# Kernel tuning notes

Measured on AMD Instinct MI355X. Metric: run time of the kernel, lower is better.

## Reference

```python
import jax, jax.numpy as jnp
import numpy as np

B, S, D = 2, 2048, 1024
NH, HD = 16, 64
MLP = 4096
EPS = 1e-6  # flax nnx.RMSNorm default epsilon


def rms_norm(x, scale):
    var = jnp.mean(jnp.square(x.astype(jnp.float32)), axis=-1, keepdims=True)
    return (x * jax.lax.rsqrt(var + EPS)).astype(x.dtype) * scale


def setup_inputs() -> dict:
    key = jax.random.key(0)
    ks = jax.random.split(key, 16)
    lin = lambda k, fin, fout: jax.random.normal(k, (fin, fout), jnp.float32) / np.sqrt(fin)
    x = jax.random.normal(ks[0], (B, S, D), jnp.float32)
    # causal mask [b, s, s]
    mask = jnp.broadcast_to(jnp.tril(jnp.ones((S, S), jnp.bool_))[None], (B, S, S))
    return {
        "x": x,
        "mask": mask,
        "attn_norm_scale": jnp.ones((D,), jnp.float32),
        "q_w": lin(ks[1], D, D), "q_b": jnp.zeros((D,), jnp.float32),
        "k_w": lin(ks[2], D, D), "k_b": jnp.zeros((D,), jnp.float32),
        "v_w": lin(ks[3], D, D), "v_b": jnp.zeros((D,), jnp.float32),
        "o_w": lin(ks[4], D, D), "o_b": jnp.zeros((D,), jnp.float32),
        "ffn_norm_scale": jnp.ones((D,), jnp.float32),
        "gate_w": lin(ks[5], D, MLP), "gate_b": jnp.zeros((MLP,), jnp.float32),
        "up_w": lin(ks[6], D, MLP), "up_b": jnp.zeros((MLP,), jnp.float32),
        "down_w": lin(ks[7], MLP, D), "down_b": jnp.zeros((D,), jnp.float32),
    }


def reference(x, mask, attn_norm_scale, q_w, q_b, k_w, k_b, v_w, v_b, o_w, o_b,
              ffn_norm_scale, gate_w, gate_b, up_w, up_b, down_w, down_b):
    b, s, d = x.shape
    h = rms_norm(x, attn_norm_scale)
    q = (h @ q_w + q_b).reshape(b, s, NH, HD)
    k = (h @ k_w + k_b).reshape(b, s, NH, HD)
    v = (h @ v_w + v_b).reshape(b, s, NH, HD)
    scale = jnp.float32(HD) ** -0.5
    logits = jnp.einsum('bsnh,btnh->bnst', q, k) * scale  # [b, n, s, s]
    logits = jnp.where(mask[:, None, :, :], logits, jnp.finfo(logits.dtype).min)
    attn = jax.nn.softmax(logits.astype(jnp.float32), axis=-1).astype(x.dtype)
    attn_out = jnp.einsum('bnst,btnh->bsnh', attn, v).reshape(b, s, d)
    x = x + attn_out @ o_w + o_b
    h = rms_norm(x, ffn_norm_scale)
    ffn = (jax.nn.silu(h @ gate_w + gate_b) * (h @ up_w + up_b)) @ down_w + down_b
    return x + ffn
```

## Files before the change

kernel.cpp:

```cpp
#include <hip/hip_runtime.h>

#define S_LEN 2048
#define DMODEL 1024
#define NHEADS 16
#define MLPDIM 4096

typedef float f32x4 __attribute__((ext_vector_type(4)));
typedef __bf16 bf16x8 __attribute__((ext_vector_type(8)));
typedef __bf16 bf16x4 __attribute__((ext_vector_type(4)));

__device__ __forceinline__ void gload_lds16(const void* gsrc, void* ldst) {
  __builtin_amdgcn_global_load_lds(
      (const __attribute__((address_space(1))) void*)gsrc,
      (__attribute__((address_space(3))) void*)ldst, 16, 0, 0);
}

#define BARR() __builtin_amdgcn_s_barrier()
#define VMC(n) do { asm volatile("s_waitcnt vmcnt(" #n ")" ::: "memory"); __builtin_amdgcn_sched_barrier(0); } while (0)

__global__ __launch_bounds__(256) void prep_k(
    const float* __restrict__ qw, const float* __restrict__ kw,
    const float* __restrict__ vw, const float* __restrict__ ow,
    const float* __restrict__ gw, const float* __restrict__ uw,
    const float* __restrict__ dw, __bf16* __restrict__ wqkv,
    __bf16* __restrict__ wo, __bf16* __restrict__ wg, __bf16* __restrict__ wu,
    __bf16* __restrict__ wd, const float* __restrict__ qb,
    const float* __restrict__ kb, const float* __restrict__ vb,
    float* __restrict__ bqkv) {
  int bid = blockIdx.x, t = threadIdx.x;
  if (bid >= 4096) {
    int i = (bid - 4096) * 256 + t;
    if (i < 1024) bqkv[i] = qb[i];
    else if (i < 2048) bqkv[i] = kb[i - 1024];
    else if (i < 3072) bqkv[i] = vb[i - 2048];
    return;
  }
  const float* in;
  __bf16* out;
  int K, N, bx, by;
  if (bid < 1024) {
    int job = bid >> 8, tt = bid & 255;
    K = 1024; N = 1024; bx = tt & 15; by = tt >> 4;
    in = (job == 0) ? qw : (job == 1) ? kw : (job == 2) ? vw : ow;
    out = (job == 0) ? wqkv : (job == 1) ? wqkv + 1024 * 1024
        : (job == 2) ? wqkv + 2 * 1024 * 1024 : wo;
  } else if (bid < 3072) {
    int job = (bid - 1024) >> 10, tt = (bid - 1024) & 1023;
    K = 1024; N = 4096; bx = tt & 63; by = tt >> 6;
    in = job ? uw : gw;
    out = job ? wu : wg;
  } else {
    int tt = bid - 3072;
    K = 4096; N = 1024; bx = tt & 15; by = tt >> 4;
    in = dw; out = wd;
  }
  __shared__ __bf16 tile[64][66];
  int n0 = bx * 64, k0 = by * 64;
  int rr = (t & 63) >> 4, sl = t & 15, wv = t >> 6;
#pragma unroll
  for (int j = 0; j < 4; ++j) {
    int r = wv * 4 + rr + j * 16;
    f32x4 v = *(const f32x4*)(in + (size_t)(k0 + r) * N + n0 + sl * 4);
#pragma unroll
    for (int e = 0; e < 4; ++e) tile[r][sl * 4 + e] = (__bf16)v[e];
  }
  __syncthreads();
#pragma unroll
  for (int j = 0; j < 2; ++j) {
    int u = t + j * 256;
    int n = u >> 3, kc = u & 7;
    bf16x8 o;
#pragma unroll
    for (int e = 0; e < 8; ++e) o[e] = tile[kc * 8 + e][n];
    *(bf16x8*)(out + (size_t)(n0 + n) * K + k0 + kc * 8) = o;
  }
}

__global__ __launch_bounds__(256) void vtrans_k(
    const __bf16* __restrict__ qkv, __bf16* __restrict__ vt) {
  __shared__ __bf16 tile[32][33];
  int s0 = blockIdx.x * 32, c0 = blockIdx.y * 32, b = blockIdx.z;
  int tx = threadIdx.x & 31, ty = threadIdx.x >> 5;
#pragma unroll
  for (int r = 0; r < 32; r += 8)
    tile[r + ty][tx] = qkv[(size_t)(b * S_LEN + s0 + r + ty) * 3072 + 2048 + c0 + tx];
  __syncthreads();
#pragma unroll
  for (int r = 0; r < 32; r += 8)
    vt[(size_t)(b * 1024 + c0 + r + ty) * S_LEN + s0 + tx] = tile[tx][r + ty];
}

__global__ __launch_bounds__(256) void rmsnorm_k(
    const float* __restrict__ x, const float* __restrict__ scale,
    __bf16* __restrict__ out) {
  int row = blockIdx.x, tid = threadIdx.x;
  f32x4 v = ((const f32x4*)(x + (size_t)row * DMODEL))[tid];
  float ss = v[0] * v[0] + v[1] * v[1] + v[2] * v[2] + v[3] * v[3];
#pragma unroll
  for (int off = 1; off < 64; off <<= 1) ss += __shfl_xor(ss, off, 64);
  __shared__ float part[4];
  if ((tid & 63) == 0) part[tid >> 6] = ss;
  __syncthreads();
  float tot = part[0] + part[1] + part[2] + part[3];
  float r = rsqrtf(tot * (1.0f / DMODEL) + 1e-6f);
  f32x4 s4 = ((const f32x4*)scale)[tid];
  bf16x4 o;
#pragma unroll
  for (int e = 0; e < 4; ++e) o[e] = (__bf16)(v[e] * r * s4[e]);
  ((bf16x4*)out)[(size_t)row * (DMODEL / 4) + tid] = o;
}

__global__ __launch_bounds__(256, 4) void gemm_gu(
    const __bf16* __restrict__ A, const __bf16* __restrict__ Gt,
    const __bf16* __restrict__ Ut, const float* __restrict__ gb,
    const float* __restrict__ ub, __bf16* __restrict__ Cout,
    int M, int N, int K) {
  __shared__ __attribute__((aligned(16))) __bf16 As[128 * 64];
  __shared__ __attribute__((aligned(16))) __bf16 Gs[64 * 64];
  __shared__ __attribute__((aligned(16))) __bf16 Us[64 * 64];
  int tid = threadIdx.x, lane = tid & 63, wave = tid >> 6;
  int l15 = lane & 15, g4 = lane >> 4;
  int lin = blockIdx.x;
  int xcd = lin & 7, idx = lin >> 3;
  int bxl = idx >> 4, byl = idx & 15;
  int bn = ((xcd & 3) * 16 + bxl) * 64;
  int bm = ((xcd >> 2) * 16 + byl) * 128;
  int wr = wave >> 1, wc = wave & 1;
  f32x4 ag[4][2] = {}, au[4][2] = {};
  const __bf16* Abase = A + (size_t)bm * K;
  const __bf16* Gbase = Gt + (size_t)bn * K;
  const __bf16* Ubase = Ut + (size_t)bn * K;

  for (int k0 = 0; k0 < K; k0 += 64) {
#pragma unroll
    for (int j = 0; j < 4; ++j) {
      int u = tid + j * 256;
      int r = u >> 3, c = (u & 7) ^ (r & 7);
      gload_lds16(Abase + (size_t)r * K + k0 + c * 8, As + u * 8);
    }
#pragma unroll
    for (int j = 0; j < 2; ++j) {
      int u = tid + j * 256;
      int r = u >> 3, c = (u & 7) ^ (r & 7);
      gload_lds16(Gbase + (size_t)r * K + k0 + c * 8, Gs + u * 8);
      gload_lds16(Ubase + (size_t)r * K + k0 + c * 8, Us + u * 8);
    }
    __syncthreads();
#pragma unroll
    for (int ks = 0; ks < 2; ++ks) {
      bf16x8 af[4], gf[2], uf[2];
#pragma unroll
      for (int m = 0; m < 4; ++m) {
        int r = wr * 64 + m * 16 + l15;
        af[m] = *(const bf16x8*)(As + r * 64 + (((4 * ks + g4) ^ (r & 7)) << 3));
      }
#pragma unroll
      for (int n = 0; n < 2; ++n) {
        int r = wc * 32 + n * 16 + l15;
        int off = r * 64 + (((4 * ks + g4) ^ (r & 7)) << 3);
        gf[n] = *(const bf16x8*)(Gs + off);
        uf[n] = *(const bf16x8*)(Us + off);
      }
      __builtin_amdgcn_s_setprio(1);
#pragma unroll
      for (int m = 0; m < 4; ++m)
#pragma unroll
        for (int n = 0; n < 2; ++n) {
          ag[m][n] = __builtin_amdgcn_mfma_f32_16x16x32_bf16(af[m], gf[n], ag[m][n], 0, 0, 0);
          au[m][n] = __builtin_amdgcn_mfma_f32_16x16x32_bf16(af[m], uf[n], au[m][n], 0, 0, 0);
        }
      __builtin_amdgcn_s_setprio(0);
    }
    __syncthreads();
  }
  int r0 = bm + wr * 64 + g4 * 4;
  int c0 = bn + wc * 32 + l15;
#pragma unroll
  for (int n = 0; n < 2; ++n) {
    int c = c0 + n * 16;
    float gbv = gb[c], ubv = ub[c];
#pragma unroll
    for (int m = 0; m < 4; ++m) {
      int rb = r0 + m * 16;
#pragma unroll
      for (int rg = 0; rg < 4; ++rg) {
        float g = ag[m][n][rg] + gbv;
        float u = au[m][n][rg] + ubv;
        float v = g / (1.0f + __expf(-g)) * u;
        Cout[(size_t)(rb + rg) * N + c] = (__bf16)v;
      }
    }
  }
}

template <int OUT_BF16, int RESID, int SILU>
__global__ __launch_bounds__(256, 3) void gemm_n64(
    const __bf16* __restrict__ A, const __bf16* __restrict__ Bt,
    const float* __restrict__ bias, const float* __restrict__ resid,
    const __bf16* __restrict__ aux, void* __restrict__ Cout,
    int M, int N, int K) {
  __shared__ __attribute__((aligned(16))) __bf16 As[2][128 * 64];
  __shared__ __attribute__((aligned(16))) __bf16 Bs[2][64 * 64];
  int tid = threadIdx.x, lane = tid & 63, wave = tid >> 6;
  int l15 = lane & 15, g4 = lane >> 4;
  int NB = N >> 6;
  int xcd = blockIdx.x & 7, j = blockIdx.x >> 3;
  int grp = j / (2 * NB), jj = j - grp * 2 * NB;
  int bm = (xcd * (M >> 10) + grp * 2 + (jj & 1)) * 128;
  int bn = (jj >> 1) * 64;
  int wr = wave >> 1, wc = wave & 1;
  f32x4 acc[4][2] = {};
  const __bf16* Abase = A + (size_t)bm * K;
  const __bf16* Bbase = Bt + (size_t)bn * K;

  auto stage = [&](int k0, int sb) {
#pragma unroll
    for (int i = 0; i < 4; ++i) {
      int u = tid + i * 256;
      int r = u >> 3, c = (u & 7) ^ (r & 7);
      gload_lds16(Abase + (size_t)r * K + k0 + c * 8, As[sb] + u * 8);
    }
#pragma unroll
    for (int i = 0; i < 2; ++i) {
      int u = tid + i * 256;
      int r = u >> 3, c = (u & 7) ^ (r & 7);
      gload_lds16(Bbase + (size_t)r * K + k0 + c * 8, Bs[sb] + u * 8);
    }
  };

  int NT = K >> 6;
  stage(0, 0);
  for (int t = 0; t < NT; ++t) {
    int sb = t & 1;
    if (t + 1 < NT) { stage((t + 1) << 6, sb ^ 1); VMC(6); }
    else { VMC(0); }
    BARR();
#pragma unroll
    for (int ks = 0; ks < 2; ++ks) {
      bf16x8 af[4], bfr[2];
#pragma unroll
      for (int m = 0; m < 4; ++m) {
        int r = wr * 64 + m * 16 + l15;
        af[m] = *(const bf16x8*)(As[sb] + r * 64 + (((4 * ks + g4) ^ (r & 7)) << 3));
      }
#pragma unroll
      for (int n = 0; n < 2; ++n) {
        int r = wc * 32 + n * 16 + l15;
        bfr[n] = *(const bf16x8*)(Bs[sb] + r * 64 + (((4 * ks + g4) ^ (r & 7)) << 3));
      }
      __builtin_amdgcn_s_setprio(1);
#pragma unroll
      for (int m = 0; m < 4; ++m)
#pragma unroll
        for (int n = 0; n < 2; ++n)
          acc[m][n] = __builtin_amdgcn_mfma_f32_16x16x32_bf16(af[m], bfr[n], acc[m][n], 0, 0, 0);
      __builtin_amdgcn_s_setprio(0);
    }
    BARR();
  }
  int r0 = bm + wr * 64 + g4 * 4;
  int c0 = bn + wc * 32 + l15;
#pragma unroll
  for (int n = 0; n < 2; ++n) {
    int c = c0 + n * 16;
    float bv = bias[c];
#pragma unroll
    for (int m = 0; m < 4; ++m) {
      int rb = r0 + m * 16;
#pragma unroll
      for (int rg = 0; rg < 4; ++rg) {
        int r = rb + rg;
        size_t idx = (size_t)r * N + c;
        float v = acc[m][n][rg] + bv;
        if (SILU) {
          float gg = (float)aux[idx];
          v *= gg / (1.0f + __expf(-gg));
        }
        if (RESID) v += resid[idx];
        if (OUT_BF16) ((__bf16*)Cout)[idx] = (__bf16)v;
        else ((float*)Cout)[idx] = v;
      }
    }
  }
}

#define SCL2E 0.180336879f
__global__ __launch_bounds__(512, 4) void attn_k(
    const __bf16* __restrict__ qkv, const __bf16* __restrict__ vt,
    __bf16* __restrict__ ao) {
  __shared__ __attribute__((aligned(16))) __bf16 Ks[2][128 * 64];
  __shared__ __attribute__((aligned(16))) __bf16 Vs[2][64 * 128];
  int tid = threadIdx.x, lane = tid & 63, w = tid >> 6;
  int l15 = lane & 15, g4 = lane >> 4;
  int bh = blockIdx.x, b = bh >> 4, h = bh & 15;
  int qt = 15 - blockIdx.y;
  int qb = qt * 128;
  int qw = qb + w * 16;
  const __bf16* qkvb = qkv + (size_t)b * S_LEN * 3072 + h * 64;
  const __bf16* kgb = qkvb + 1024;
  const __bf16* vtb = vt + (size_t)b * 1024 * S_LEN + (size_t)(h * 64) * S_LEN;

  bf16x8 qf[2];
#pragma unroll
  for (int ks = 0; ks < 2; ++ks)
    qf[ks] = *(const bf16x8*)(qkvb + (size_t)(qw + l15) * 3072 + 32 * ks + 8 * g4);

  f32x4 oa[4] = {};
  float mrow = -1e30f, lrow = 0.f;
  int q = qw + l15;
  int nt = qt + 1;

  auto stage = [&](int kvb, int buf) {
#pragma unroll
    for (int i = 0; i < 2; ++i) {
      int u = tid + i * 512;
      int r = u >> 3, c = u & 7;
      gload_lds16(kgb + (size_t)(kvb + r) * 3072 + ((c ^ (r & 7)) << 3),
                  Ks[buf] + w * 512 + i * 4096);
    }
#pragma unroll
    for (int i = 0; i < 2; ++i) {
      int u = tid + i * 512;
      int r = u >> 4, cu = u & 15;
      gload_lds16(vtb + (size_t)r * S_LEN + kvb + ((cu ^ (r & 7)) << 3),
                  Vs[buf] + w * 512 + i * 4096);
    }
  };

  stage(0, 0);
  __syncthreads();
  int buf = 0;
  for (int t = 0; t < nt; ++t) {
    int kvb = t * 128;
    if (t + 1 < nt) stage(kvb + 128, buf ^ 1);

    f32x4 sa[8];
#pragma unroll
    for (int i = 0; i < 8; ++i) sa[i] = f32x4{0.f, 0.f, 0.f, 0.f};
#pragma unroll
    for (int st = 0; st < 2; ++st)
#pragma unroll
      for (int ks = 0; ks < 2; ++ks) {
        bf16x8 kf[4];
#pragma unroll
        for (int n = 0; n < 4; ++n) {
          int rr = st * 64 + n * 16 + l15;
          int bc = (64 * ks + 16 * g4) ^ ((rr & 7) << 4);
          kf[n] = *(const bf16x8*)((const char*)Ks[buf] + rr * 128 + bc);
        }
        __builtin_amdgcn_s_setprio(1);
#pragma unroll
        for (int n = 0; n < 4; ++n)
          sa[st * 4 + n] = __builtin_amdgcn_mfma_f32_16x16x32_bf16(kf[n], qf[ks], sa[st * 4 + n], 0, 0, 0);
        __builtin_amdgcn_s_setprio(0);
      }

    bool lastt = (t == nt - 1);
    float nmx = -1e30f;
#pragma unroll
    for (int i = 0; i < 8; ++i)
#pragma unroll
      for (int rg = 0; rg < 4; ++rg) {
        float s = sa[i][rg] * SCL2E;
        if (lastt) {
          int key = kvb + (i >> 2) * 64 + (i & 3) * 16 + 4 * g4 + rg;
          s = (key <= q) ? s : -1e30f;
        }
        sa[i][rg] = s;
        nmx = fmaxf(nmx, s);
      }
    nmx = fmaxf(nmx, __shfl_xor(nmx, 16));
    nmx = fmaxf(nmx, __shfl_xor(nmx, 32));
    float nm;
    if (!__all(nmx <= mrow)) {
      nm = fmaxf(mrow, nmx);
      float sc = exp2f(mrow - nm);
      mrow = nm;
      lrow *= sc;
#pragma unroll
      for (int rg = 0; rg < 4; ++rg) {
        float scq = __shfl(sc, 4 * g4 + rg);
#pragma unroll
        for (int dn = 0; dn < 4; ++dn) oa[dn][rg] *= scq;
      }
    } else {
      nm = mrow;
    }
    float rs = 0.f;
    bf16x8 pa[2][2];
#pragma unroll
    for (int st = 0; st < 2; ++st)
#pragma unroll
      for (int ks = 0; ks < 2; ++ks)
#pragma unroll
        for (int hf = 0; hf < 2; ++hf)
#pragma unroll
          for (int rg = 0; rg < 4; ++rg) {
            float p = exp2f(sa[st * 4 + 2 * ks + hf][rg] - nm);
            rs += p;
            pa[st][ks][hf * 4 + rg] = (__bf16)p;
          }
    rs += __shfl_xor(rs, 16);
    rs += __shfl_xor(rs, 32);
    lrow += rs;

#pragma unroll
    for (int st = 0; st < 2; ++st)
#pragma unroll
      for (int ks = 0; ks < 2; ++ks) {
        __builtin_amdgcn_s_setprio(1);
#pragma unroll
        for (int dn = 0; dn < 4; ++dn) {
          int rr = dn * 16 + l15;
          int swz = (rr & 7) << 4;
          int bb = st * 128 + 64 * ks + 8 * g4;
          const char* vrow = (const char*)Vs[buf] + rr * 256;
          bf16x4 v0 = *(const bf16x4*)(vrow + (bb ^ swz));
          bf16x4 v1 = *(const bf16x4*)(vrow + ((bb + 32) ^ swz));
          bf16x8 vf;
          vf[0] = v0[0]; vf[1] = v0[1]; vf[2] = v0[2]; vf[3] = v0[3];
          vf[4] = v1[0]; vf[5] = v1[1]; vf[6] = v1[2]; vf[7] = v1[3];
          oa[dn] = __builtin_amdgcn_mfma_f32_16x16x32_bf16(pa[st][ks], vf, oa[dn], 0, 0, 0);
        }
        __builtin_amdgcn_s_setprio(0);
      }
    __syncthreads();
    buf ^= 1;
  }

  __bf16* aobase = ao + (size_t)b * S_LEN * DMODEL + h * 64;
#pragma unroll
  for (int rg = 0; rg < 4; ++rg) {
    float rl = 1.0f / __shfl(lrow, 4 * g4 + rg);
    int qo = qw + 4 * g4 + rg;
#pragma unroll
    for (int dn = 0; dn < 4; ++dn)
      aobase[(size_t)qo * DMODEL + dn * 16 + l15] = (__bf16)(oa[dn][rg] * rl);
  }
}

#define OFF_WQKV 0
#define OFF_WO 6291456
#define OFF_WG 8388608
#define OFF_WU 16777216
#define OFF_WD 25165824
#define OFF_BQKV 33554432
#define OFF_H 33570816
#define OFF_QKV 41959424
#define OFF_AO 67125248
#define OFF_T 75513856
#define OFF_VT OFF_T
#define OFF_X2 109068288

extern "C" void kernel_launch(void* const* d_in, const int* in_sizes, int n_in,
                              void* d_out, int out_size, void* d_ws, size_t ws_size,
                              hipStream_t stream) {
  (void)in_sizes; (void)n_in; (void)out_size; (void)ws_size;
  const float* x = (const float*)d_in[0];
  const float* attn_scale = (const float*)d_in[2];
  const float* q_w = (const float*)d_in[3];
  const float* q_b = (const float*)d_in[4];
  const float* k_w = (const float*)d_in[5];
  const float* k_b = (const float*)d_in[6];
  const float* v_w = (const float*)d_in[7];
  const float* v_b = (const float*)d_in[8];
  const float* o_w = (const float*)d_in[9];
  const float* o_b = (const float*)d_in[10];
  const float* ffn_scale = (const float*)d_in[11];
  const float* gate_w = (const float*)d_in[12];
  const float* gate_b = (const float*)d_in[13];
  const float* up_w = (const float*)d_in[14];
  const float* up_b = (const float*)d_in[15];
  const float* down_w = (const float*)d_in[16];
  const float* down_b = (const float*)d_in[17];

  char* ws = (char*)d_ws;
  __bf16* wqkv = (__bf16*)(ws + OFF_WQKV);
  __bf16* wo = (__bf16*)(ws + OFF_WO);
  __bf16* wg = (__bf16*)(ws + OFF_WG);
  __bf16* wu = (__bf16*)(ws + OFF_WU);
  __bf16* wd = (__bf16*)(ws + OFF_WD);
  float* bqkv = (float*)(ws + OFF_BQKV);
  __bf16* hbuf = (__bf16*)(ws + OFF_H);
  __bf16* qkvbuf = (__bf16*)(ws + OFF_QKV);
  __bf16* aobuf = (__bf16*)(ws + OFF_AO);
  __bf16* tbuf = (__bf16*)(ws + OFF_T);
  __bf16* vtbuf = (__bf16*)(ws + OFF_VT);
  float* x2 = (float*)(ws + OFF_X2);

  dim3 blk(256);
  prep_k<<<dim3(4108), blk, 0, stream>>>(q_w, k_w, v_w, o_w, gate_w, up_w, down_w,
                                         wqkv, wo, wg, wu, wd, q_b, k_b, v_b, bqkv);
  rmsnorm_k<<<4096, blk, 0, stream>>>(x, attn_scale, hbuf);
  gemm_n64<1, 0, 0><<<dim3(1536), blk, 0, stream>>>(hbuf, wqkv, bqkv, nullptr, nullptr, qkvbuf, 4096, 3072, 1024);
  vtrans_k<<<dim3(64, 32, 2), blk, 0, stream>>>(qkvbuf, vtbuf);
  attn_k<<<dim3(32, 16), dim3(512), 0, stream>>>(qkvbuf, vtbuf, aobuf);
  gemm_n64<0, 1, 0><<<dim3(512), blk, 0, stream>>>(aobuf, wo, o_b, x, nullptr, x2, 4096, 1024, 1024);
  rmsnorm_k<<<4096, blk, 0, stream>>>(x2, ffn_scale, hbuf);
  gemm_gu<<<dim3(2048), blk, 0, stream>>>(hbuf, wg, wu, gate_b, up_b, tbuf, 4096, 4096, 1024);
  gemm_n64<0, 1, 0><<<dim3(512), blk, 0, stream>>>(tbuf, wd, down_b, x2, nullptr, (float*)d_out, 4096, 1024, 4096);
}
```

Before: 257.0 us.

## Fold first RMSNorm into prep kernel and permute V transpose for wide LDS reads

The attention RMSNorm is merged into the weight-prep launch as extra blocks, which removes one kernel launch and lets the norm run alongside the weight conversion. Separately, the V-transpose kernel now writes keys in a permuted order so that the attention kernel can fetch each 8-element V fragment with a single 16-byte LDS read instead of two 8-byte reads plus register shuffling. The permutation has to match the MFMA operand layout exactly, or the P·V products will be wrong.

```diff
diff --git a/kernel.cpp b/kernel.cpp
--- a/kernel.cpp
+++ b/kernel.cpp
@@ -26,13 +26,33 @@
     __bf16* __restrict__ wo, __bf16* __restrict__ wg, __bf16* __restrict__ wu,
     __bf16* __restrict__ wd, const float* __restrict__ qb,
     const float* __restrict__ kb, const float* __restrict__ vb,
-    float* __restrict__ bqkv) {
+    float* __restrict__ bqkv, const float* __restrict__ x,
+    const float* __restrict__ ascale, __bf16* __restrict__ hbuf) {
+  __shared__ __bf16 tile[64][66];
+  __shared__ float part[4];
   int bid = blockIdx.x, t = threadIdx.x;
-  if (bid >= 4096) {
-    int i = (bid - 4096) * 256 + t;
+  if (bid >= 8192) {
+    int i = (bid - 8192) * 256 + t;
     if (i < 1024) bqkv[i] = qb[i];
     else if (i < 2048) bqkv[i] = kb[i - 1024];
     else if (i < 3072) bqkv[i] = vb[i - 2048];
+    return;
+  }
+  if (bid >= 4096) {
+    int row = bid - 4096;
+    f32x4 v = ((const f32x4*)(x + (size_t)row * DMODEL))[t];
+    float ss = v[0] * v[0] + v[1] * v[1] + v[2] * v[2] + v[3] * v[3];
+#pragma unroll
+    for (int off = 1; off < 64; off <<= 1) ss += __shfl_xor(ss, off, 64);
+    if ((t & 63) == 0) part[t >> 6] = ss;
+    __syncthreads();
+    float tot = part[0] + part[1] + part[2] + part[3];
+    float r = rsqrtf(tot * (1.0f / DMODEL) + 1e-6f);
+    f32x4 s4 = ((const f32x4*)ascale)[t];
+    bf16x4 o;
+#pragma unroll
+    for (int e = 0; e < 4; ++e) o[e] = (__bf16)(v[e] * r * s4[e]);
+    ((bf16x4*)hbuf)[(size_t)row * (DMODEL / 4) + t] = o;
     return;
   }
   const float* in;
@@ -54,7 +74,6 @@
     K = 4096; N = 1024; bx = tt & 15; by = tt >> 4;
     in = dw; out = wd;
   }
-  __shared__ __bf16 tile[64][66];
   int n0 = bx * 64, k0 = by * 64;
   int rr = (t & 63) >> 4, sl = t & 15, wv = t >> 6;
 #pragma unroll
@@ -85,9 +104,11 @@
   for (int r = 0; r < 32; r += 8)
     tile[r + ty][tx] = qkv[(size_t)(b * S_LEN + s0 + r + ty) * 3072 + 2048 + c0 + tx];
   __syncthreads();
+  int hf = (tx >> 4) & 1, g4q = (tx >> 2) & 3, r2 = tx & 3;
+  int txp = g4q * 8 + hf * 4 + r2;
 #pragma unroll
   for (int r = 0; r < 32; r += 8)
-    vt[(size_t)(b * 1024 + c0 + r + ty) * S_LEN + s0 + tx] = tile[tx][r + ty];
+    vt[(size_t)(b * 1024 + c0 + r + ty) * S_LEN + s0 + txp] = tile[tx][r + ty];
 }
 
 __global__ __launch_bounds__(256) void rmsnorm_k(
@@ -413,13 +434,8 @@
         for (int dn = 0; dn < 4; ++dn) {
           int rr = dn * 16 + l15;
           int swz = (rr & 7) << 4;
-          int bb = st * 128 + 64 * ks + 8 * g4;
           const char* vrow = (const char*)Vs[buf] + rr * 256;
-          bf16x4 v0 = *(const bf16x4*)(vrow + (bb ^ swz));
-          bf16x4 v1 = *(const bf16x4*)(vrow + ((bb + 32) ^ swz));
-          bf16x8 vf;
-          vf[0] = v0[0]; vf[1] = v0[1]; vf[2] = v0[2]; vf[3] = v0[3];
-          vf[4] = v1[0]; vf[5] = v1[1]; vf[6] = v1[2]; vf[7] = v1[3];
+          bf16x8 vf = *(const bf16x8*)(vrow + ((st * 128 + ks * 64 + g4 * 16) ^ swz));
           oa[dn] = __builtin_amdgcn_mfma_f32_16x16x32_bf16(pa[st][ks], vf, oa[dn], 0, 0, 0);
         }
         __builtin_amdgcn_s_setprio(0);
@@ -489,9 +505,9 @@
   float* x2 = (float*)(ws + OFF_X2);
 
   dim3 blk(256);
-  prep_k<<<dim3(4108), blk, 0, stream>>>(q_w, k_w, v_w, o_w, gate_w, up_w, down_w,
-                                         wqkv, wo, wg, wu, wd, q_b, k_b, v_b, bqkv);
-  rmsnorm_k<<<4096, blk, 0, stream>>>(x, attn_scale, hbuf);
+  prep_k<<<dim3(8204), blk, 0, stream>>>(q_w, k_w, v_w, o_w, gate_w, up_w, down_w,
+                                         wqkv, wo, wg, wu, wd, q_b, k_b, v_b, bqkv,
+                                         x, attn_scale, hbuf);
   gemm_n64<1, 0, 0><<<dim3(1536), blk, 0, stream>>>(hbuf, wqkv, bqkv, nullptr, nullptr, qkvbuf, 4096, 3072, 1024);
   vtrans_k<<<dim3(64, 32, 2), blk, 0, stream>>>(qkvbuf, vtbuf);
   attn_k<<<dim3(32, 16), dim3(512), 0, stream>>>(qkvbuf, vtbuf, aobuf);
```

After: 250.5 us. -2.5%, faster.
